# Kernel tuning notes

Hardware: AMD Instinct MI355X
Metric: run time of the kernel (lower is better)

Reference implementation:

```python
import jax, jax.numpy as jnp
import numpy as np

BN_EPS = 1e-5
N_NODES = 250000
C_IN = 32
C_OUT = 32
K = 27  # 3x3x3 octree stencil


def setup_inputs() -> dict:
    key = jax.random.key(0)
    k1, k2, k3 = jax.random.split(key, 3)
    x = jax.random.normal(k1, (N_NODES, C_IN), dtype=jnp.float32)
    neigh = jax.random.randint(k2, (N_NODES, K), 0, N_NODES, dtype=jnp.int32)
    # fan-in style init for the conv weight
    weight = jax.random.normal(k3, (K, C_IN, C_OUT), dtype=jnp.float32) / np.sqrt(K * C_IN)
    bn_gamma = jnp.ones((C_OUT,), dtype=jnp.float32)
    bn_beta = jnp.zeros((C_OUT,), dtype=jnp.float32)
    return {"x": x, "neigh": neigh, "weight": weight,
            "bn_gamma": bn_gamma, "bn_beta": bn_beta}


def reference(x, neigh, weight, bn_gamma, bn_beta):
    # --- OctreeConv: gather 27 neighbors per node, contract with weight ---
    g = x[neigh]  # [N, K, Cin] irregular gather
    y = jnp.einsum('nkc,kcd->nd', g, weight)  # [N, Cout]
    # --- BatchNorm1d (training mode: batch statistics, biased variance) ---
    mean = jnp.mean(y, axis=0)
    var = jnp.mean(jnp.square(y - mean), axis=0)
    yn = (y - mean) * jax.lax.rsqrt(var + BN_EPS) * bn_gamma + bn_beta
    # --- ELU ---
    return jax.nn.elu(yn)
```

## Files before the change

kernel.cpp:

```cpp
#include <hip/hip_runtime.h>
#include <hip/hip_bf16.h>
#include <math.h>

#define NN 250000
#define CIN 32
#define COUT 32
#define KK 27
#define BN_EPS 1e-5f

typedef __attribute__((ext_vector_type(8))) short bf16x8;
typedef __attribute__((ext_vector_type(4))) float f32x4;

#define WS_WB_OFF   512
#define WS_XB_OFF   65536
#define WS_NEED     (WS_XB_OFF + (size_t)NN * CIN * 2)

static __device__ __forceinline__ unsigned short f2bf(float f) {
    unsigned int u = __float_as_uint(f);
    unsigned int r = (u + 0x7fffu + ((u >> 16) & 1u)) >> 16;
    return (unsigned short)r;
}

__global__ __launch_bounds__(256) void convert_x_kernel(
    const float* __restrict__ x, unsigned short* __restrict__ xb)
{
    size_t i = (size_t)blockIdx.x * 256 + threadIdx.x;
    size_t total = (size_t)NN * CIN / 8;
    if (i >= total) return;
    const float4* xp = (const float4*)x;
    float4 a = xp[i * 2], b = xp[i * 2 + 1];
    union { unsigned short u[8]; uint4 v; } o;
    o.u[0] = f2bf(a.x); o.u[1] = f2bf(a.y); o.u[2] = f2bf(a.z); o.u[3] = f2bf(a.w);
    o.u[4] = f2bf(b.x); o.u[5] = f2bf(b.y); o.u[6] = f2bf(b.z); o.u[7] = f2bf(b.w);
    ((uint4*)xb)[i] = o.v;
}

__global__ __launch_bounds__(256) void pack_w_kernel(
    const float* __restrict__ w, unsigned short* __restrict__ wbp)
{
    int tid = blockIdx.x * 256 + threadIdx.x;
    if (tid >= KK * 2 * 64 * 8) return;
    int j = tid & 7;
    int l = (tid >> 3) & 63;
    int h = (tid >> 9) & 1;
    int k = tid >> 10;
    int c = (l >> 4) * 8 + j;
    int d = h * 16 + (l & 15);
    wbp[tid] = f2bf(w[k * (CIN * COUT) + c * COUT + d]);
}

__global__ __launch_bounds__(256) void conv_mfma_kernel(
    const unsigned short* __restrict__ xb,
    const int* __restrict__ neigh,
    const unsigned short* __restrict__ wbp,
    float* __restrict__ y)
{
    __shared__ int lidx[64 * KK];
    int b0 = blockIdx.x * 64;
    for (int t = threadIdx.x; t < 64 * KK; t += 256) {
        long long g = (long long)b0 * KK + t;
        lidx[t] = (g < (long long)NN * KK) ? neigh[g] : 0;
    }
    __syncthreads();

    int lane = threadIdx.x & 63;
    int wid  = threadIdx.x >> 6;
    int row  = lane & 15;
    int grp  = lane >> 4;
    int nl   = wid * 16 + row;

    f32x4 acc0 = {0.f, 0.f, 0.f, 0.f};
    f32x4 acc1 = {0.f, 0.f, 0.f, 0.f};
    const bf16x8* wb = (const bf16x8*)wbp;

#pragma unroll
    for (int k = 0; k < KK; ++k) {
        int nidx = lidx[nl * KK + k];
        bf16x8 a = *(const bf16x8*)(xb + (size_t)nidx * CIN + grp * 8);
        bf16x8 bb0 = wb[(k * 2 + 0) * 64 + lane];
        bf16x8 bb1 = wb[(k * 2 + 1) * 64 + lane];
        acc0 = __builtin_amdgcn_mfma_f32_16x16x32_bf16(a, bb0, acc0, 0, 0, 0);
        acc1 = __builtin_amdgcn_mfma_f32_16x16x32_bf16(a, bb1, acc1, 0, 0, 0);
    }

    int base = b0 + wid * 16;
#pragma unroll
    for (int i = 0; i < 4; ++i) {
        int node = base + grp * 4 + i;
        if (node < NN) {
            y[(size_t)node * COUT + (lane & 15)]      = acc0[i];
            y[(size_t)node * COUT + 16 + (lane & 15)] = acc1[i];
        }
    }
}

__global__ __launch_bounds__(256) void conv_kernel(
    const float* __restrict__ x, const int* __restrict__ neigh,
    const float* __restrict__ w, float* __restrict__ y)
{
    int n = blockIdx.x * 256 + threadIdx.x;
    bool valid = (n < NN);
    int nsafe = valid ? n : 0;
    int idx[KK];
#pragma unroll
    for (int k = 0; k < KK; ++k) idx[k] = neigh[(size_t)nsafe * KK + k];
    float acc[COUT];
#pragma unroll
    for (int d = 0; d < COUT; ++d) acc[d] = 0.0f;
    for (int k = 0; k < KK; ++k) {
        const float4* xr = (const float4*)(x + (size_t)idx[k] * CIN);
        float4 xv[8];
#pragma unroll
        for (int j = 0; j < 8; ++j) xv[j] = xr[j];
        const float* wk = w + k * (CIN * COUT);
        const float* xs = (const float*)xv;
#pragma unroll
        for (int c = 0; c < CIN; ++c) {
            float xc = xs[c];
#pragma unroll
            for (int d = 0; d < COUT; ++d)
                acc[d] = fmaf(xc, wk[c * COUT + d], acc[d]);
        }
    }
    if (valid) {
        float4* yr = (float4*)(y + (size_t)n * COUT);
#pragma unroll
        for (int j = 0; j < 8; ++j) {
            float4 v;
            v.x = acc[j*4+0]; v.y = acc[j*4+1]; v.z = acc[j*4+2]; v.w = acc[j*4+3];
            yr[j] = v;
        }
    }
}

__global__ __launch_bounds__(256) void stats_kernel(
    const float* __restrict__ y, float* __restrict__ ws)
{
    int d = threadIdx.x & 31;
    int rib = threadIdx.x >> 5;
    float s = 0.0f, q = 0.0f;
    for (int r = blockIdx.x * 8 + rib; r < NN; r += gridDim.x * 8) {
        float v = y[(size_t)r * COUT + d];
        s += v;
        q += v * v;
    }
    __shared__ float ls[8][32];
    __shared__ float lq[8][32];
    ls[rib][d] = s;
    lq[rib][d] = q;
    __syncthreads();
    if (threadIdx.x < 32) {
        float S = 0.0f, Q = 0.0f;
#pragma unroll
        for (int i = 0; i < 8; ++i) { S += ls[i][threadIdx.x]; Q += lq[i][threadIdx.x]; }
        atomicAdd(&ws[threadIdx.x], S);
        atomicAdd(&ws[32 + threadIdx.x], Q);
    }
}

__global__ void finalize_kernel(
    const float* __restrict__ gamma, const float* __restrict__ beta,
    float* __restrict__ ws)
{
    int d = threadIdx.x;
    if (d < 32) {
        float invN = 1.0f / (float)NN;
        float mean = ws[d] * invN;
        float var = ws[32 + d] * invN - mean * mean;
        float rstd = rsqrtf(var + BN_EPS);
        float scale = rstd * gamma[d];
        ws[64 + d] = scale;
        ws[96 + d] = beta[d] - mean * scale;
    }
}

__global__ __launch_bounds__(256) void bn_elu_kernel(
    float* __restrict__ y, const float* __restrict__ ws)
{
    __shared__ float sc[32], sh[32];
    if (threadIdx.x < 32) {
        sc[threadIdx.x] = ws[64 + threadIdx.x];
        sh[threadIdx.x] = ws[96 + threadIdx.x];
    }
    __syncthreads();
    size_t i = (size_t)blockIdx.x * 256 + threadIdx.x;
    size_t total = (size_t)NN * COUT / 4;
    if (i >= total) return;
    int c0 = (int)((i * 4) & 31);
    float4 v = ((const float4*)y)[i];
    float r[4] = {v.x, v.y, v.z, v.w};
#pragma unroll
    for (int j = 0; j < 4; ++j) {
        float t = r[j] * sc[c0 + j] + sh[c0 + j];
        r[j] = (t > 0.0f) ? t : expm1f(t);
    }
    float4 o; o.x = r[0]; o.y = r[1]; o.z = r[2]; o.w = r[3];
    ((float4*)y)[i] = o;
}

extern "C" void kernel_launch(void* const* d_in, const int* in_sizes, int n_in,
                              void* d_out, int out_size, void* d_ws, size_t ws_size,
                              hipStream_t stream) {
    const float* x     = (const float*)d_in[0];
    const int*   neigh = (const int*)d_in[1];
    const float* w     = (const float*)d_in[2];
    const float* gamma = (const float*)d_in[3];
    const float* beta  = (const float*)d_in[4];
    float* y  = (float*)d_out;
    float* ws = (float*)d_ws;

    hipMemsetAsync(ws, 0, 512, stream);

    if (ws_size >= WS_NEED) {
        unsigned short* wbp = (unsigned short*)((char*)d_ws + WS_WB_OFF);
        unsigned short* xb  = (unsigned short*)((char*)d_ws + WS_XB_OFF);

        size_t cvt_total = (size_t)NN * CIN / 8;
        convert_x_kernel<<<(int)((cvt_total + 255) / 256), 256, 0, stream>>>(x, xb);
        pack_w_kernel<<<(KK * 2 * 64 * 8 + 255) / 256, 256, 0, stream>>>(w, wbp);

        int convBlocks = (NN + 63) / 64;
        conv_mfma_kernel<<<convBlocks, 256, 0, stream>>>(xb, neigh, wbp, y);
    } else {
        int convBlocks = (NN + 255) / 256;
        conv_kernel<<<convBlocks, 256, 0, stream>>>(x, neigh, w, y);
    }

    stats_kernel<<<512, 256, 0, stream>>>(y, ws);
    finalize_kernel<<<1, 32, 0, stream>>>(gamma, beta, ws);

    size_t total4 = (size_t)NN * COUT / 4;
    bn_elu_kernel<<<(int)((total4 + 255) / 256), 256, 0, stream>>>(y, ws);
}
```

Baseline: 160.6 us.

## Fuse BN stats into MFMA conv, pipeline gathers, merge prep kernels

The x-convert and weight-pack kernels are merged into one prep launch. The MFMA conv kernel now handles 32 nodes per wave (two 16-row tiles). It drops the shared-memory index staging in favour of a software-pipelined, double-buffered schedule: neighbour indices load two groups ahead and bf16 gathers one group ahead of the MFMAs. Per-channel sum and sum-of-squares are reduced inside the conv epilogue with shuffles, shared memory and atomics, which removes the separate stats pass over y. The trade-off is higher register pressure, capped with launch_bounds(256,3), and more float atomics.

After: 160.3 us. Within noise of the previous version (-0.2%).

```diff
diff --git a/kernel.cpp b/kernel.cpp
--- a/kernel.cpp
+++ b/kernel.cpp
@@ -15,82 +15,147 @@
 #define WS_XB_OFF   65536
 #define WS_NEED     (WS_XB_OFF + (size_t)NN * CIN * 2)
 
+#define CVT_CHUNKS  ((NN * CIN) / 8)
+#define CVT_BLOCKS  ((CVT_CHUNKS + 255) / 256)
+#define PACK_ELEMS  (KK * 2 * 64 * 8)
+#define PACK_BLOCKS ((PACK_ELEMS + 255) / 256)
+
 static __device__ __forceinline__ unsigned short f2bf(float f) {
     unsigned int u = __float_as_uint(f);
     unsigned int r = (u + 0x7fffu + ((u >> 16) & 1u)) >> 16;
     return (unsigned short)r;
 }
 
-__global__ __launch_bounds__(256) void convert_x_kernel(
-    const float* __restrict__ x, unsigned short* __restrict__ xb)
-{
-    size_t i = (size_t)blockIdx.x * 256 + threadIdx.x;
-    size_t total = (size_t)NN * CIN / 8;
-    if (i >= total) return;
-    const float4* xp = (const float4*)x;
-    float4 a = xp[i * 2], b = xp[i * 2 + 1];
-    union { unsigned short u[8]; uint4 v; } o;
-    o.u[0] = f2bf(a.x); o.u[1] = f2bf(a.y); o.u[2] = f2bf(a.z); o.u[3] = f2bf(a.w);
-    o.u[4] = f2bf(b.x); o.u[5] = f2bf(b.y); o.u[6] = f2bf(b.z); o.u[7] = f2bf(b.w);
-    ((uint4*)xb)[i] = o.v;
-}
-
-__global__ __launch_bounds__(256) void pack_w_kernel(
+__global__ __launch_bounds__(256) void prep_kernel(
+    const float* __restrict__ x, unsigned short* __restrict__ xb,
     const float* __restrict__ w, unsigned short* __restrict__ wbp)
 {
-    int tid = blockIdx.x * 256 + threadIdx.x;
-    if (tid >= KK * 2 * 64 * 8) return;
-    int j = tid & 7;
-    int l = (tid >> 3) & 63;
-    int h = (tid >> 9) & 1;
-    int k = tid >> 10;
-    int c = (l >> 4) * 8 + j;
-    int d = h * 16 + (l & 15);
-    wbp[tid] = f2bf(w[k * (CIN * COUT) + c * COUT + d]);
-}
-
-__global__ __launch_bounds__(256) void conv_mfma_kernel(
+    int b = blockIdx.x;
+    if (b < CVT_BLOCKS) {
+        size_t i = (size_t)b * 256 + threadIdx.x;
+        if (i >= CVT_CHUNKS) return;
+        const float4* xp = (const float4*)x;
+        float4 a = xp[i * 2], c = xp[i * 2 + 1];
+        union { unsigned short u[8]; uint4 v; } o;
+        o.u[0] = f2bf(a.x); o.u[1] = f2bf(a.y); o.u[2] = f2bf(a.z); o.u[3] = f2bf(a.w);
+        o.u[4] = f2bf(c.x); o.u[5] = f2bf(c.y); o.u[6] = f2bf(c.z); o.u[7] = f2bf(c.w);
+        ((uint4*)xb)[i] = o.v;
+    } else {
+        int tid = (b - CVT_BLOCKS) * 256 + threadIdx.x;
+        if (tid >= PACK_ELEMS) return;
+        int j = tid & 7;
+        int l = (tid >> 3) & 63;
+        int h = (tid >> 9) & 1;
+        int k = tid >> 10;
+        int c = (l >> 4) * 8 + j;
+        int d = h * 16 + (l & 15);
+        wbp[tid] = f2bf(w[k * (CIN * COUT) + c * COUT + d]);
+    }
+}
+
+__global__ __launch_bounds__(256, 3) void conv_mfma_kernel(
     const unsigned short* __restrict__ xb,
     const int* __restrict__ neigh,
     const unsigned short* __restrict__ wbp,
-    float* __restrict__ y)
-{
-    __shared__ int lidx[64 * KK];
-    int b0 = blockIdx.x * 64;
-    for (int t = threadIdx.x; t < 64 * KK; t += 256) {
-        long long g = (long long)b0 * KK + t;
-        lidx[t] = (g < (long long)NN * KK) ? neigh[g] : 0;
-    }
-    __syncthreads();
-
+    float* __restrict__ y,
+    float* __restrict__ ws)
+{
     int lane = threadIdx.x & 63;
     int wid  = threadIdx.x >> 6;
-    int row  = lane & 15;
+    int col  = lane & 15;
     int grp  = lane >> 4;
-    int nl   = wid * 16 + row;
-
-    f32x4 acc0 = {0.f, 0.f, 0.f, 0.f};
-    f32x4 acc1 = {0.f, 0.f, 0.f, 0.f};
-    const bf16x8* wb = (const bf16x8*)wbp;
-
-#pragma unroll
-    for (int k = 0; k < KK; ++k) {
-        int nidx = lidx[nl * KK + k];
-        bf16x8 a = *(const bf16x8*)(xb + (size_t)nidx * CIN + grp * 8);
-        bf16x8 bb0 = wb[(k * 2 + 0) * 64 + lane];
-        bf16x8 bb1 = wb[(k * 2 + 1) * 64 + lane];
-        acc0 = __builtin_amdgcn_mfma_f32_16x16x32_bf16(a, bb0, acc0, 0, 0, 0);
-        acc1 = __builtin_amdgcn_mfma_f32_16x16x32_bf16(a, bb1, acc1, 0, 0, 0);
-    }
-
-    int base = b0 + wid * 16;
-#pragma unroll
-    for (int i = 0; i < 4; ++i) {
-        int node = base + grp * 4 + i;
-        if (node < NN) {
-            y[(size_t)node * COUT + (lane & 15)]      = acc0[i];
-            y[(size_t)node * COUT + 16 + (lane & 15)] = acc1[i];
+
+    int base = blockIdx.x * 128 + wid * 32;
+    int nd[2];
+#pragma unroll
+    for (int t = 0; t < 2; ++t) {
+        int n = base + t * 16 + col;
+        nd[t] = (n < NN) ? n : (NN - 1);
+    }
+
+    const bf16x8* wbv = (const bf16x8*)wbp;
+
+    int    vidx[2][3][2];
+    bf16x8 va[2][3][2];
+    bf16x8 vb[2][3][2];
+    f32x4  acc[2][2];
+#pragma unroll
+    for (int t = 0; t < 2; ++t)
+#pragma unroll
+        for (int h = 0; h < 2; ++h) acc[t][h] = (f32x4){0.f, 0.f, 0.f, 0.f};
+
+#define S0(BUF, G) do {                                                          \
+    _Pragma("unroll") for (int kk = 0; kk < 3; ++kk) {                           \
+        _Pragma("unroll") for (int t = 0; t < 2; ++t)                            \
+            vidx[BUF][kk][t] = neigh[(size_t)nd[t] * KK + (G) * 3 + kk];         \
+    } } while (0)
+
+#define S1(BUF, G) do {                                                          \
+    _Pragma("unroll") for (int kk = 0; kk < 3; ++kk) {                           \
+        _Pragma("unroll") for (int t = 0; t < 2; ++t)                            \
+            va[BUF][kk][t] = *(const bf16x8*)(xb + (size_t)vidx[BUF][kk][t] * CIN + grp * 8); \
+        _Pragma("unroll") for (int h = 0; h < 2; ++h)                            \
+            vb[BUF][kk][h] = wbv[(((G) * 3 + kk) * 2 + h) * 64 + lane];          \
+    } } while (0)
+
+#define CG(BUF, G) do {                                                          \
+    _Pragma("unroll") for (int kk = 0; kk < 3; ++kk) {                           \
+        _Pragma("unroll") for (int t = 0; t < 2; ++t) {                          \
+            _Pragma("unroll") for (int h = 0; h < 2; ++h)                        \
+                acc[t][h] = __builtin_amdgcn_mfma_f32_16x16x32_bf16(             \
+                    va[BUF][kk][t], vb[BUF][kk][h], acc[t][h], 0, 0, 0);         \
+        }                                                                        \
+    } } while (0)
+
+    S0(0, 0); S1(0, 0); S0(1, 1);
+    S1(1, 1); S0(0, 2); CG(0, 0);
+    S1(0, 2); S0(1, 3); CG(1, 1);
+    S1(1, 3); S0(0, 4); CG(0, 2);
+    S1(0, 4); S0(1, 5); CG(1, 3);
+    S1(1, 5); S0(0, 6); CG(0, 4);
+    S1(0, 6); S0(1, 7); CG(1, 5);
+    S1(1, 7); S0(0, 8); CG(0, 6);
+    S1(0, 8);           CG(1, 7);
+                        CG(0, 8);
+
+#undef S0
+#undef S1
+#undef CG
+
+    float s0 = 0.f, q0 = 0.f, s1 = 0.f, q1 = 0.f;
+#pragma unroll
+    for (int t = 0; t < 2; ++t) {
+#pragma unroll
+        for (int i = 0; i < 4; ++i) {
+            int node = base + t * 16 + grp * 4 + i;
+            float v0 = acc[t][0][i], v1 = acc[t][1][i];
+            if (node < NN) {
+                y[(size_t)node * COUT + col]      = v0;
+                y[(size_t)node * COUT + 16 + col] = v1;
+                s0 += v0; q0 += v0 * v0;
+                s1 += v1; q1 += v1 * v1;
+            }
         }
+    }
+    s0 += __shfl_xor(s0, 16); s0 += __shfl_xor(s0, 32);
+    q0 += __shfl_xor(q0, 16); q0 += __shfl_xor(q0, 32);
+    s1 += __shfl_xor(s1, 16); s1 += __shfl_xor(s1, 32);
+    q1 += __shfl_xor(q1, 16); q1 += __shfl_xor(q1, 32);
+
+    __shared__ float sred[4][2][16];
+    __shared__ float qred[4][2][16];
+    if (lane < 16) {
+        sred[wid][0][col] = s0; qred[wid][0][col] = q0;
+        sred[wid][1][col] = s1; qred[wid][1][col] = q1;
+    }
+    __syncthreads();
+    if (threadIdx.x < 32) {
+        int h = threadIdx.x >> 4, c = threadIdx.x & 15;
+        float S = 0.f, Q = 0.f;
+#pragma unroll
+        for (int wv = 0; wv < 4; ++wv) { S += sred[wv][h][c]; Q += qred[wv][h][c]; }
+        atomicAdd(&ws[h * 16 + c], S);
+        atomicAdd(&ws[32 + h * 16 + c], Q);
     }
 }
 
@@ -215,18 +280,16 @@
         unsigned short* wbp = (unsigned short*)((char*)d_ws + WS_WB_OFF);
         unsigned short* xb  = (unsigned short*)((char*)d_ws + WS_XB_OFF);
 
-        size_t cvt_total = (size_t)NN * CIN / 8;
-        convert_x_kernel<<<(int)((cvt_total + 255) / 256), 256, 0, stream>>>(x, xb);
-        pack_w_kernel<<<(KK * 2 * 64 * 8 + 255) / 256, 256, 0, stream>>>(w, wbp);
-
-        int convBlocks = (NN + 63) / 64;
-        conv_mfma_kernel<<<convBlocks, 256, 0, stream>>>(xb, neigh, wbp, y);
+        prep_kernel<<<CVT_BLOCKS + PACK_BLOCKS, 256, 0, stream>>>(x, xb, w, wbp);
+
+        int convBlocks = (NN + 127) / 128;
+        conv_mfma_kernel<<<convBlocks, 256, 0, stream>>>(xb, neigh, wbp, y, ws);
     } else {
         int convBlocks = (NN + 255) / 256;
         conv_kernel<<<convBlocks, 256, 0, stream>>>(x, neigh, w, y);
-    }
-
-    stats_kernel<<<512, 256, 0, stream>>>(y, ws);
+        stats_kernel<<<512, 256, 0, stream>>>(y, ws);
+    }
+
     finalize_kernel<<<1, 32, 0, stream>>>(gamma, beta, ws);
 
     size_t total4 = (size_t)NN * COUT / 4;
```
